# Kernel optimization log

Hardware: AMD Instinct MI355X
Metric: run time of the kernel (lower is better)

Reference implementation:

```python
import jax, jax.numpy as jnp
import numpy as np

MIN = 1      # window length; module's squeeze-based assignment requires min == 1
STRIDE = 10
NUM_FEATURES = 64

# precompute upper-triangular pair indices (i < j), row-major -> matches the
# nested (i, j) loop ordering of the torch module
_PAIR_I, _PAIR_J = np.triu_indices(NUM_FEATURES, k=1)
_PAIR_I = jnp.asarray(_PAIR_I)
_PAIR_J = jnp.asarray(_PAIR_J)


def setup_inputs() -> dict:
    key = jax.random.key(0)
    x = jax.random.normal(key, (256, NUM_FEATURES, 2000), dtype=jnp.float32)
    return {"x": x}


def reference(x):
    # x: [B, F, T]
    B, F, T = x.shape
    out_T = (T - MIN) // STRIDE + 1
    # strided sample of window starts: [B, F, out_T]
    sampled = x[:, :, : out_T * STRIDE : STRIDE]
    # pairwise channel differences, upper triangle: [B, F*(F-1)//2, out_T]
    return sampled[:, _PAIR_I, :] - sampled[:, _PAIR_J, :]
```

## Files before the change

### kernel.cpp

```cpp
#include <hip/hip_runtime.h>


#define NF     64
#define T_OUT  200
#define NPAIR  2016
#define NB     256
#define RF4    500
#define TV4    50
#define NT     1024

typedef float fx4 __attribute__((ext_vector_type(4)));

__global__ __launch_bounds__(NT)
void ts_sub_b(const fx4* __restrict__ xv, fx4* __restrict__ out) {
    __shared__ __attribute__((aligned(16))) float sf[NF * T_OUT];
    __shared__ unsigned char pi[NPAIR];
    __shared__ unsigned char pj[NPAIR];

    const int tid = threadIdx.x;
    const int b   = blockIdx.x;

    for (int p = tid; p < NPAIR; p += NT) {
        float d = 16129.0f - 8.0f * (float)p;
        int i = (int)((127.0f - sqrtf(d)) * 0.5f);
        if (i < 0) i = 0;
        while (i > 0 && (i * (127 - i)) / 2 > p) --i;
        while (((i + 1) * (126 - i)) / 2 <= p) ++i;
        pi[p] = (unsigned char)i;
        pj[p] = (unsigned char)(p - (i * (127 - i)) / 2 + i + 1);
    }

    {
        const fx4* __restrict__ xb = xv + (size_t)b * (NF * RF4);
        int row = tid / T_OUT;
        int k   = tid - row * T_OUT;
        for (int idx = tid; idx < NF * T_OUT; idx += NT) {
            fx4 v = __builtin_nontemporal_load(
                        &xb[row * RF4 + 5 * (k >> 1) + 2 * (k & 1)]);
            sf[row * T_OUT + k] = (k & 1) ? v.z : v.x;
            row += 5;
            k += 24;
            if (k >= T_OUT) { k -= T_OUT; ++row; }
        }
    }
    __syncthreads();

    const fx4* __restrict__ s4 = reinterpret_cast<const fx4*>(sf);
    fx4* __restrict__ ob = out + (size_t)b * (NPAIR * TV4);

    int p  = tid / TV4;
    int t4 = tid - p * TV4;
    for (int v = tid; v < NPAIR * TV4; v += NT) {
        fx4 a = s4[pi[p] * TV4 + t4];
        fx4 c = s4[pj[p] * TV4 + t4];
        fx4 r = a - c;
        __builtin_nontemporal_store(r, &ob[(size_t)p * TV4 + t4]);
        p += 20;
        t4 += 24;
        if (t4 >= TV4) { t4 -= TV4; ++p; }
    }
}

extern "C" void kernel_launch(void* const* d_in, const int* in_sizes, int n_in,
                              void* d_out, int out_size, void* d_ws, size_t ws_size,
                              hipStream_t stream) {
    const float* x = (const float*)d_in[0];
    float* out = (float*)d_out;
    ts_sub_b<<<dim3(NB), dim3(NT), 0, stream>>>((const fx4*)x, (fx4*)out);
}
```

Baseline: 101.2 us.

## Split time axis into halves and overlap second-half LDS loads with first-half stores

Stages the strided input into two LDS buffers, one per half of the output time axis, using direct global-to-LDS loads. The second half's loads are issued before the first half's pair-difference stores, so the load latency is meant to be hidden behind the store phase. In exchange, each pair row is written as two 400-byte segments in separate passes, and scalar strided loads replace the wider vector loads.

```diff
diff --git a/kernel.cpp b/kernel.cpp
--- a/kernel.cpp
+++ b/kernel.cpp
@@ -2,23 +2,29 @@
 
 
 #define NF     64
-#define T_OUT  200
+#define T_IN   2000
 #define NPAIR  2016
 #define NB     256
-#define RF4    500
 #define TV4    50
+#define HV4    25
 #define NT     1024
+#define HALF   (NF * 100)
 
 typedef float fx4 __attribute__((ext_vector_type(4)));
+typedef __attribute__((address_space(3))) float       lds_f32;
+typedef __attribute__((address_space(1))) const float  g_f32;
 
 __global__ __launch_bounds__(NT)
-void ts_sub_b(const fx4* __restrict__ xv, fx4* __restrict__ out) {
-    __shared__ __attribute__((aligned(16))) float sf[NF * T_OUT];
+void ts_sub_pipe(const float* __restrict__ xf, fx4* __restrict__ out) {
+    __shared__ __attribute__((aligned(16))) float bufA[HALF];
+    __shared__ __attribute__((aligned(16))) float bufB[HALF];
     __shared__ unsigned char pi[NPAIR];
     __shared__ unsigned char pj[NPAIR];
 
-    const int tid = threadIdx.x;
-    const int b   = blockIdx.x;
+    const int tid  = threadIdx.x;
+    const int lane = tid & 63;
+    const int b    = blockIdx.x;
+    const float* __restrict__ xb = xf + (size_t)b * (NF * T_IN);
 
     for (int p = tid; p < NPAIR; p += NT) {
         float d = 16129.0f - 8.0f * (float)p;
@@ -30,34 +36,59 @@
         pj[p] = (unsigned char)(p - (i * (127 - i)) / 2 + i + 1);
     }
 
-    {
-        const fx4* __restrict__ xb = xv + (size_t)b * (NF * RF4);
-        int row = tid / T_OUT;
-        int k   = tid - row * T_OUT;
-        for (int idx = tid; idx < NF * T_OUT; idx += NT) {
-            fx4 v = __builtin_nontemporal_load(
-                        &xb[row * RF4 + 5 * (k >> 1) + 2 * (k & 1)]);
-            sf[row * T_OUT + k] = (k & 1) ? v.z : v.x;
-            row += 5;
-            k += 24;
-            if (k >= T_OUT) { k -= T_OUT; ++row; }
+    #pragma unroll
+    for (int it = 0; it < 7; ++it) {
+        int idx = it * NT + tid;
+        if (idx < HALF) {
+            int row = idx / 100;
+            int kk  = idx - row * 100;
+            __builtin_amdgcn_global_load_lds(
+                (g_f32*)(xb + row * T_IN + kk * 10),
+                (lds_f32*)(bufA + (idx - lane)), 4, 0, 0);
         }
     }
     __syncthreads();
 
-    const fx4* __restrict__ s4 = reinterpret_cast<const fx4*>(sf);
+    #pragma unroll
+    for (int it = 0; it < 7; ++it) {
+        int idx = it * NT + tid;
+        if (idx < HALF) {
+            int row = idx / 100;
+            int kk  = idx - row * 100;
+            __builtin_amdgcn_global_load_lds(
+                (g_f32*)(xb + row * T_IN + 1000 + kk * 10),
+                (lds_f32*)(bufB + (idx - lane)), 4, 0, 0);
+        }
+    }
+
+    const fx4* __restrict__ sA = reinterpret_cast<const fx4*>(bufA);
     fx4* __restrict__ ob = out + (size_t)b * (NPAIR * TV4);
+    {
+        int p  = tid / HV4;
+        int tl = tid - p * HV4;
+        for (int v = tid; v < NPAIR * HV4; v += NT) {
+            fx4 a = sA[pi[p] * HV4 + tl];
+            fx4 c = sA[pj[p] * HV4 + tl];
+            __builtin_nontemporal_store(a - c, &ob[(size_t)p * TV4 + tl]);
+            p += 40;
+            tl += 24;
+            if (tl >= HV4) { tl -= HV4; ++p; }
+        }
+    }
+    __syncthreads();
 
-    int p  = tid / TV4;
-    int t4 = tid - p * TV4;
-    for (int v = tid; v < NPAIR * TV4; v += NT) {
-        fx4 a = s4[pi[p] * TV4 + t4];
-        fx4 c = s4[pj[p] * TV4 + t4];
-        fx4 r = a - c;
-        __builtin_nontemporal_store(r, &ob[(size_t)p * TV4 + t4]);
-        p += 20;
-        t4 += 24;
-        if (t4 >= TV4) { t4 -= TV4; ++p; }
+    const fx4* __restrict__ sB = reinterpret_cast<const fx4*>(bufB);
+    {
+        int p  = tid / HV4;
+        int tl = tid - p * HV4;
+        for (int v = tid; v < NPAIR * HV4; v += NT) {
+            fx4 a = sB[pi[p] * HV4 + tl];
+            fx4 c = sB[pj[p] * HV4 + tl];
+            __builtin_nontemporal_store(a - c, &ob[(size_t)p * TV4 + HV4 + tl]);
+            p += 40;
+            tl += 24;
+            if (tl >= HV4) { tl -= HV4; ++p; }
+        }
     }
 }
 
@@ -66,5 +97,5 @@
                               hipStream_t stream) {
     const float* x = (const float*)d_in[0];
     float* out = (float*)d_out;
-    ts_sub_b<<<dim3(NB), dim3(NT), 0, stream>>>((const fx4*)x, (fx4*)out);
+    ts_sub_pipe<<<dim3(NB), dim3(NT), 0, stream>>>(x, (fx4*)out);
 }
```

Measured after the change: 188.3 us. 86.1% more time.

## Pipeline input loads in feature chunks overlapped with pair-difference stores

Applied to the files above, without the earlier changes.

Splits the 64 feature rows into four chunks of 16 and reorders the pair list so that pairs whose rows are all loaded can be written as soon as each chunk arrives. The global loads for the next chunk are issued into registers before the current chunk's pairs are emitted, so input read latency overlaps with the output store stream. A remapped pair table gives each pair's output row. This adds register pressure (16 fx4 live values), extra syncs, and a scattered output row order within each block.

```diff
diff --git a/kernel.cpp b/kernel.cpp
--- a/kernel.cpp
+++ b/kernel.cpp
@@ -8,57 +8,116 @@
 #define RF4    500
 #define TV4    50
 #define NT     1024
+#define CH     3200
 
 typedef float fx4 __attribute__((ext_vector_type(4)));
 
 __global__ __launch_bounds__(NT)
-void ts_sub_b(const fx4* __restrict__ xv, fx4* __restrict__ out) {
+void ts_sub_pipe(const fx4* __restrict__ xv, fx4* __restrict__ out) {
     __shared__ __attribute__((aligned(16))) float sf[NF * T_OUT];
-    __shared__ unsigned char pi[NPAIR];
-    __shared__ unsigned char pj[NPAIR];
+    __shared__ unsigned char  ir[NPAIR];
+    __shared__ unsigned char  jr[NPAIR];
+    __shared__ unsigned short obr[NPAIR];
 
     const int tid = threadIdx.x;
     const int b   = blockIdx.x;
+    const fx4* __restrict__ xb = xv + (size_t)b * (NF * RF4);
+    fx4* __restrict__ ob = out + (size_t)b * (NPAIR * TV4);
+    const fx4* __restrict__ s4 = reinterpret_cast<const fx4*>(sf);
 
-    for (int p = tid; p < NPAIR; p += NT) {
-        float d = 16129.0f - 8.0f * (float)p;
-        int i = (int)((127.0f - sqrtf(d)) * 0.5f);
-        if (i < 0) i = 0;
-        while (i > 0 && (i * (127 - i)) / 2 > p) --i;
-        while (((i + 1) * (126 - i)) / 2 <= p) ++i;
-        pi[p] = (unsigned char)i;
-        pj[p] = (unsigned char)(p - (i * (127 - i)) / 2 + i + 1);
+#define ISSUE(C, R0, R1, R2, R3)                                              \
+    {                                                                         \
+        int l = tid;                                                          \
+        { int r = l / 200, k = l - 200 * r;                                   \
+          R0 = __builtin_nontemporal_load(                                    \
+                   &xb[(16*(C)+r)*RF4 + 5*(k>>1) + 2*(k&1)]); }               \
+        l += NT;                                                              \
+        { int r = l / 200, k = l - 200 * r;                                   \
+          R1 = __builtin_nontemporal_load(                                    \
+                   &xb[(16*(C)+r)*RF4 + 5*(k>>1) + 2*(k&1)]); }               \
+        l += NT;                                                              \
+        { int r = l / 200, k = l - 200 * r;                                   \
+          R2 = __builtin_nontemporal_load(                                    \
+                   &xb[(16*(C)+r)*RF4 + 5*(k>>1) + 2*(k&1)]); }               \
+        l += NT;                                                              \
+        if (l < CH) { int r = l / 200, k = l - 200 * r;                       \
+          R3 = __builtin_nontemporal_load(                                    \
+                   &xb[(16*(C)+r)*RF4 + 5*(k>>1) + 2*(k&1)]); }               \
     }
 
-    {
-        const fx4* __restrict__ xb = xv + (size_t)b * (NF * RF4);
-        int row = tid / T_OUT;
-        int k   = tid - row * T_OUT;
-        for (int idx = tid; idx < NF * T_OUT; idx += NT) {
-            fx4 v = __builtin_nontemporal_load(
-                        &xb[row * RF4 + 5 * (k >> 1) + 2 * (k & 1)]);
-            sf[row * T_OUT + k] = (k & 1) ? v.z : v.x;
-            row += 5;
-            k += 24;
-            if (k >= T_OUT) { k -= T_OUT; ++row; }
+#define EXTRACT(C, R0, R1, R2, R3)                                            \
+    {                                                                         \
+        int l = tid;                                                          \
+        sf[(C)*CH + l] = (l & 1) ? R0.z : R0.x;  l += NT;                     \
+        sf[(C)*CH + l] = (l & 1) ? R1.z : R1.x;  l += NT;                     \
+        sf[(C)*CH + l] = (l & 1) ? R2.z : R2.x;  l += NT;                     \
+        if (l < CH) sf[(C)*CH + l] = (l & 1) ? R3.z : R3.x;                   \
+    }
+
+#define EMIT(OFFC, NC)                                                        \
+    {                                                                         \
+        int p  = tid / TV4;                                                   \
+        int t4 = tid - p * TV4;                                               \
+        for (int v = tid; v < (NC) * TV4; v += NT) {                          \
+            int g = (OFFC) + p;                                               \
+            fx4 A  = s4[ir[g] * TV4 + t4];                                    \
+            fx4 Cc = s4[jr[g] * TV4 + t4];                                    \
+            __builtin_nontemporal_store(A - Cc,                               \
+                &ob[(size_t)obr[g] * TV4 + t4]);                              \
+            p += 20; t4 += 24;                         \
+            if (t4 >= TV4) { t4 -= TV4; ++p; }                                \
+        }                                                                     \
+    }
+
+    fx4 a0{}, a1{}, a2{}, a3{}, b0{}, b1{}, b2{}, b3{};
+    fx4 c0{}, c1{}, c2{}, c3{}, d0{}, d1{}, d2{}, d3{};
+
+    ISSUE(0, a0, a1, a2, a3)
+
+    for (int g = tid; g < NPAIR; g += NT) {
+        int c = (g < 120) ? 0 : (g < 496) ? 1 : (g < 1128) ? 2 : 3;
+        int e = g - ((c == 0) ? 0 : (c == 1) ? 120 : (c == 2) ? 496 : 1128);
+        int i, j;
+        if (e < 256 * c) {
+            i = e >> 4;
+            j = 16 * c + (e & 15);
+        } else {
+            int f = e - 256 * c, iloc = 0;
+            while (f >= 15 - iloc) { f -= 15 - iloc; ++iloc; }
+            i = 16 * c + iloc;
+            j = i + 1 + f;
         }
+        ir[g]  = (unsigned char)i;
+        jr[g]  = (unsigned char)j;
+        obr[g] = (unsigned short)(i * (127 - i) / 2 + (j - i - 1));
     }
+
+    EXTRACT(0, a0, a1, a2, a3)
     __syncthreads();
 
-    const fx4* __restrict__ s4 = reinterpret_cast<const fx4*>(sf);
-    fx4* __restrict__ ob = out + (size_t)b * (NPAIR * TV4);
+    ISSUE(1, b0, b1, b2, b3)
+    __builtin_amdgcn_sched_barrier(0);
+    EMIT(0, 120)
+    EXTRACT(1, b0, b1, b2, b3)
+    __syncthreads();
 
-    int p  = tid / TV4;
-    int t4 = tid - p * TV4;
-    for (int v = tid; v < NPAIR * TV4; v += NT) {
-        fx4 a = s4[pi[p] * TV4 + t4];
-        fx4 c = s4[pj[p] * TV4 + t4];
-        fx4 r = a - c;
-        __builtin_nontemporal_store(r, &ob[(size_t)p * TV4 + t4]);
-        p += 20;
-        t4 += 24;
-        if (t4 >= TV4) { t4 -= TV4; ++p; }
-    }
+    ISSUE(2, c0, c1, c2, c3)
+    __builtin_amdgcn_sched_barrier(0);
+    EMIT(120, 376)
+    EXTRACT(2, c0, c1, c2, c3)
+    __syncthreads();
+
+    ISSUE(3, d0, d1, d2, d3)
+    __builtin_amdgcn_sched_barrier(0);
+    EMIT(496, 632)
+    EXTRACT(3, d0, d1, d2, d3)
+    __syncthreads();
+
+    EMIT(1128, 888)
+
+#undef ISSUE
+#undef EXTRACT
+#undef EMIT
 }
 
 extern "C" void kernel_launch(void* const* d_in, const int* in_sizes, int n_in,
@@ -66,5 +125,5 @@
                               hipStream_t stream) {
     const float* x = (const float*)d_in[0];
     float* out = (float*)d_out;
-    ts_sub_b<<<dim3(NB), dim3(NT), 0, stream>>>((const fx4*)x, (fx4*)out);
+    ts_sub_pipe<<<dim3(NB), dim3(NT), 0, stream>>>((const fx4*)x, (fx4*)out);
 }
```

New measurement: 124.6 us. 1.23x slower.

## Split block into producer/consumer waves with per-chunk LDS flags

Applied to the files above, without the earlier changes.

The block is split into 256 producer threads that load the strided input into LDS in four 16-row chunks and 768 consumer threads that compute pair differences. Consumers spin on workgroup-scope atomic flags, so each chunk's output pairs, those whose i and j lie in loaded rows, can be written while later rows are still loading. Pair indices are regrouped by chunk, with a remap table giving each pair's output row. The aim is to overlap the input load latency with the output store stream, at the cost of fewer threads issuing loads, spin-wait overhead and scattered output rows.

```diff
diff --git a/kernel.cpp b/kernel.cpp
--- a/kernel.cpp
+++ b/kernel.cpp
@@ -8,56 +8,89 @@
 #define RF4    500
 #define TV4    50
 #define NT     1024
+#define CH     3200
+#define NCONS  768
 
 typedef float fx4 __attribute__((ext_vector_type(4)));
 
 __global__ __launch_bounds__(NT)
-void ts_sub_b(const fx4* __restrict__ xv, fx4* __restrict__ out) {
+void ts_sub_pc(const fx4* __restrict__ xv, fx4* __restrict__ out) {
     __shared__ __attribute__((aligned(16))) float sf[NF * T_OUT];
-    __shared__ unsigned char pi[NPAIR];
-    __shared__ unsigned char pj[NPAIR];
+    __shared__ unsigned char  ir[NPAIR];
+    __shared__ unsigned char  jr[NPAIR];
+    __shared__ unsigned short obr[NPAIR];
+    __shared__ int flags[4];
 
     const int tid = threadIdx.x;
     const int b   = blockIdx.x;
+    const fx4* __restrict__ xb = xv + (size_t)b * (NF * RF4);
 
-    for (int p = tid; p < NPAIR; p += NT) {
-        float d = 16129.0f - 8.0f * (float)p;
-        int i = (int)((127.0f - sqrtf(d)) * 0.5f);
-        if (i < 0) i = 0;
-        while (i > 0 && (i * (127 - i)) / 2 > p) --i;
-        while (((i + 1) * (126 - i)) / 2 <= p) ++i;
-        pi[p] = (unsigned char)i;
-        pj[p] = (unsigned char)(p - (i * (127 - i)) / 2 + i + 1);
-    }
-
-    {
-        const fx4* __restrict__ xb = xv + (size_t)b * (NF * RF4);
-        int row = tid / T_OUT;
-        int k   = tid - row * T_OUT;
-        for (int idx = tid; idx < NF * T_OUT; idx += NT) {
-            fx4 v = __builtin_nontemporal_load(
-                        &xb[row * RF4 + 5 * (k >> 1) + 2 * (k & 1)]);
-            sf[row * T_OUT + k] = (k & 1) ? v.z : v.x;
-            row += 5;
-            k += 24;
-            if (k >= T_OUT) { k -= T_OUT; ++row; }
-        }
-    }
+    if (tid < 4) flags[tid] = 0;
     __syncthreads();
 
-    const fx4* __restrict__ s4 = reinterpret_cast<const fx4*>(sf);
-    fx4* __restrict__ ob = out + (size_t)b * (NPAIR * TV4);
+    if (tid < 256) {
+        for (int c = 0; c < 4; ++c) {
+            int rl = 0, k = tid;
+            if (k >= T_OUT) { rl = 1; k -= T_OUT; }
+            const int rbase = 16 * c;
+            #pragma unroll
+            for (int it = 0; it < 13; ++it) {
+                if (it < 12 || tid < 128) {
+                    fx4 v = __builtin_nontemporal_load(
+                        &xb[(rbase + rl) * RF4 + 5 * (k >> 1) + 2 * (k & 1)]);
+                    sf[c * CH + it * 256 + tid] = (k & 1) ? v.z : v.x;
+                }
+                rl += 1; k += 56;
+                if (k >= T_OUT) { k -= T_OUT; ++rl; }
+            }
+            if ((tid & 63) == 0)
+                __hip_atomic_fetch_add(&flags[c], 1, __ATOMIC_RELEASE,
+                                       __HIP_MEMORY_SCOPE_WORKGROUP);
+        }
+    } else {
+        const int ctid = tid - 256;
 
-    int p  = tid / TV4;
-    int t4 = tid - p * TV4;
-    for (int v = tid; v < NPAIR * TV4; v += NT) {
-        fx4 a = s4[pi[p] * TV4 + t4];
-        fx4 c = s4[pj[p] * TV4 + t4];
-        fx4 r = a - c;
-        __builtin_nontemporal_store(r, &ob[(size_t)p * TV4 + t4]);
-        p += 20;
-        t4 += 24;
-        if (t4 >= TV4) { t4 -= TV4; ++p; }
+        for (int g = ctid; g < NPAIR; g += NCONS) {
+            int c = (g < 120) ? 0 : (g < 496) ? 1 : (g < 1128) ? 2 : 3;
+            int e = g - ((c == 0) ? 0 : (c == 1) ? 120 : (c == 2) ? 496 : 1128);
+            int i, j;
+            if (e < 256 * c) {
+                i = e >> 4;
+                j = 16 * c + (e & 15);
+            } else {
+                int f = e - 256 * c, iloc = 0;
+                while (f >= 15 - iloc) { f -= 15 - iloc; ++iloc; }
+                i = 16 * c + iloc;
+                j = i + 1 + f;
+            }
+            ir[g]  = (unsigned char)i;
+            jr[g]  = (unsigned char)j;
+            obr[g] = (unsigned short)(i * (127 - i) / 2 + (j - i - 1));
+        }
+
+        const fx4* __restrict__ s4 = reinterpret_cast<const fx4*>(sf);
+        fx4* __restrict__ ob = out + (size_t)b * (NPAIR * TV4);
+        const int off[4] = {0, 120, 496, 1128};
+        const int cnt[4] = {120, 376, 632, 888};
+
+        for (int c = 0; c < 4; ++c) {
+            while (__hip_atomic_load(&flags[c], __ATOMIC_ACQUIRE,
+                                     __HIP_MEMORY_SCOPE_WORKGROUP) < 4)
+                __builtin_amdgcn_s_sleep(4);
+
+            const int OFFC = off[c], NC = cnt[c];
+            int p  = ctid / TV4;
+            int t4 = ctid - p * TV4;
+            for (int v = ctid; v < NC * TV4; v += NCONS) {
+                int g = OFFC + p;
+                fx4 A  = s4[ir[g] * TV4 + t4];
+                fx4 Cc = s4[jr[g] * TV4 + t4];
+                __builtin_nontemporal_store(A - Cc,
+                    &ob[(size_t)obr[g] * TV4 + t4]);
+                p += 15; t4 += 18;
+                if (t4 >= TV4) { t4 -= TV4; ++p; }
+            }
+        }
     }
 }
 
@@ -66,5 +99,5 @@
                               hipStream_t stream) {
     const float* x = (const float*)d_in[0];
     float* out = (float*)d_out;
-    ts_sub_b<<<dim3(NB), dim3(NT), 0, stream>>>((const fx4*)x, (fx4*)out);
+    ts_sub_pc<<<dim3(NB), dim3(NT), 0, stream>>>((const fx4*)x, (fx4*)out);
 }
```

Measured after the change: 127.6 us. 26.1% more time.
